# Performance work log

Measured on AMD Instinct MI355X. Metric: run time of the kernel, lower is better.

## Reference

```python
import jax, jax.numpy as jnp
import numpy as np

ALPHA = 1.0  # alpha hyperparameter; sigma=None and module in training mode with
# track_running_stats=True -> first-call behavior: sigma_square = alpha * mean(d2.detach())

def setup_inputs() -> dict:
    key = jax.random.key(0)
    X = jax.random.normal(key, (8192, 512), dtype=jnp.float32)
    return {"X": X}

def reference(X):
    # Pairwise squared L2 distances via ||xi||^2 + ||xj||^2 - 2 xi.xj (GEMM trick)
    sq = jnp.sum(X * X, axis=1)                      # [m]
    gram = X @ X.T                                   # [m, m]
    d2 = sq[:, None] + sq[None, :] - 2.0 * gram      # [m, m]
    d2 = jnp.maximum(d2, 0.0)                        # numerical safety
    sigma_square = ALPHA * jnp.mean(jax.lax.stop_gradient(d2))
    return jnp.exp(-d2 / (2.0 * sigma_square))
```

## Files before the change

kernel.cpp:

```cpp
#include <hip/hip_runtime.h>
#include <stdint.h>
#include <math.h>

#define MROWS 8192
#define KDIM  512

typedef __attribute__((ext_vector_type(8))) short short8;
typedef __attribute__((ext_vector_type(4))) float f32x4;

#if __has_builtin(__builtin_amdgcn_exp2f)
#define EXP2F(x) __builtin_amdgcn_exp2f(x)
#else
#define EXP2F(x) exp2f(x)
#endif

#define GL2LDS(gp, lp) __builtin_amdgcn_global_load_lds( \
    (__attribute__((address_space(1))) void*)(gp),       \
    (__attribute__((address_space(3))) void*)(lp), 16, 0, 0)

__device__ inline unsigned short f2bf_rne(float f) {
  unsigned u = __builtin_bit_cast(unsigned, f);
  unsigned r = 0x7FFFu + ((u >> 16) & 1u);
  return (unsigned short)((u + r) >> 16);
}

__device__ inline int swzP(int row, int g) {
  return (row * 4) ^ (g ^ (row & 3)) ^ (((row >> 2) & 1) << 2);
}

__global__ __launch_bounds__(512) void k_prep(
    const float* __restrict__ X, unsigned short* __restrict__ Xb,
    float* __restrict__ sq, float* __restrict__ svec_part,
    float* __restrict__ sumsq_part) {
  __shared__ float ssv[8][512];
  __shared__ float ssq[8];
  const int tid = threadIdx.x, lane = tid & 63, w = tid >> 6;
  const int b = blockIdx.x;

  float ca[8] = {0.f, 0.f, 0.f, 0.f, 0.f, 0.f, 0.f, 0.f};
  float lss = 0.f;

  for (int rr = 0; rr < 4; ++rr) {
    const int row = b * 32 + w * 4 + rr;
    const float4* xr = (const float4*)(X + (size_t)row * KDIM);
    float4 v0 = xr[lane];
    float4 v1 = xr[64 + lane];

    ushort4 p0, p1;
    p0.x = f2bf_rne(v0.x); p0.y = f2bf_rne(v0.y);
    p0.z = f2bf_rne(v0.z); p0.w = f2bf_rne(v0.w);
    p1.x = f2bf_rne(v1.x); p1.y = f2bf_rne(v1.y);
    p1.z = f2bf_rne(v1.z); p1.w = f2bf_rne(v1.w);
    *(ushort4*)(Xb + (size_t)row * KDIM + lane * 4)       = p0;
    *(ushort4*)(Xb + (size_t)row * KDIM + 256 + lane * 4) = p1;

    float s2 = v0.x*v0.x + v0.y*v0.y + v0.z*v0.z + v0.w*v0.w
             + v1.x*v1.x + v1.y*v1.y + v1.z*v1.z + v1.w*v1.w;
    float rs = s2;
#pragma unroll
    for (int off = 32; off; off >>= 1) rs += __shfl_xor(rs, off, 64);
    if (lane == 0) sq[row] = rs;
    lss += s2;

    ca[0] += v0.x; ca[1] += v0.y; ca[2] += v0.z; ca[3] += v0.w;
    ca[4] += v1.x; ca[5] += v1.y; ca[6] += v1.z; ca[7] += v1.w;
  }

#pragma unroll
  for (int i = 0; i < 4; ++i) {
    ssv[w][lane * 4 + i]       = ca[i];
    ssv[w][256 + lane * 4 + i] = ca[4 + i];
  }
  float wsum = lss;
#pragma unroll
  for (int off = 32; off; off >>= 1) wsum += __shfl_xor(wsum, off, 64);
  if (lane == 0) ssq[w] = wsum;
  __syncthreads();

  float s = 0.f;
#pragma unroll
  for (int ww = 0; ww < 8; ++ww) s += ssv[ww][tid];
  svec_part[(size_t)b * 512 + tid] = s;
  if (tid == 0)
    sumsq_part[b] = ssq[0] + ssq[1] + ssq[2] + ssq[3] +
                    ssq[4] + ssq[5] + ssq[6] + ssq[7];
}

__global__ __launch_bounds__(512) void k_sig_a(
    const float* __restrict__ svec_part, const float* __restrict__ sumsq_part,
    float* __restrict__ svec2, float* __restrict__ sumsq2) {
  const int tid = threadIdx.x, b = blockIdx.x;
  float s = 0.f;
#pragma unroll
  for (int k = 0; k < 4; ++k)
    s += svec_part[(size_t)(b * 4 + k) * 512 + tid];
  svec2[(size_t)b * 512 + tid] = s;
  if (tid == 0)
    sumsq2[b] = sumsq_part[b * 4] + sumsq_part[b * 4 + 1] +
                sumsq_part[b * 4 + 2] + sumsq_part[b * 4 + 3];
}

__global__ __launch_bounds__(256) void k_sigma(
    const float* __restrict__ svec2, const float* __restrict__ sumsq2,
    float* __restrict__ scale) {
  __shared__ float red[4];
  const int tid = threadIdx.x, lane = tid & 63, w = tid >> 6;
  float s1 = 0.f, s2 = 0.f;
#pragma unroll 4
  for (int b = 0; b < 64; ++b) {
    s1 += svec2[(size_t)b * 512 + tid];
    s2 += svec2[(size_t)b * 512 + 256 + tid];
  }
  float ss = s1 * s1 + s2 * s2;
#pragma unroll
  for (int off = 32; off; off >>= 1) ss += __shfl_xor(ss, off, 64);
  if (lane == 0) red[w] = ss;
  __syncthreads();
  if (tid == 0) {
    float sst = red[0] + red[1] + red[2] + red[3];
    float sumsq = 0.f;
#pragma unroll
    for (int b = 0; b < 64; ++b) sumsq += sumsq2[b];
    const float m = (float)MROWS;
    float meand2 = 2.f * sumsq / m - 2.f * sst / (m * m);
    float sigma2 = 1.0f * meand2;
    scale[0] = 1.4426950408889634f / (2.f * sigma2);
  }
}

__global__ __launch_bounds__(256, 3) void k_gemm(
    const unsigned short* __restrict__ Xb, const float* __restrict__ sq,
    const float* __restrict__ scale, float* __restrict__ out) {
  __shared__ __align__(16) char smem[49152];
  unsigned short* Asm = (unsigned short*)smem;
  unsigned short* Bsm = (unsigned short*)(smem + 24576);
  float* tr = (float*)smem;

  const int tid = threadIdx.x, lane = tid & 63, w = tid >> 6;
  const int wr = w >> 1, wc = w & 1;
  const int ln15 = lane & 15, g = lane >> 4;

  const int blk = blockIdx.x;
  const int r = (blk & 7) * 260 + (blk >> 3);
  int bi, bj;
  if (r < 1536) {
    const int sp = r >> 8;
    const int inner = r & 255;
    const int SI = (sp < 3) ? 0 : ((sp < 5) ? 1 : 2);
    const int SJ = (sp < 3) ? sp + 1 : ((sp < 5) ? sp - 1 : 3);
    bi = SI * 16 + (inner & 15);
    bj = SJ * 16 + (inner >> 4);
  } else {
    const int rd = r - 1536;
    const int sd = rd / 136;
    const int k = rd - sd * 136;
    int b = (int)((sqrtf(8.0f * (float)k + 1.0f) - 1.0f) * 0.5f);
    while ((b + 1) * (b + 2) / 2 <= k) ++b;
    while (b * (b + 1) / 2 > k) --b;
    const int a = k - b * (b + 1) / 2;
    bi = sd * 16 + a;
    bj = sd * 16 + b;
  }

  const unsigned short* XbA = Xb + (size_t)bi * 128 * KDIM;
  const unsigned short* XbB = Xb + (size_t)bj * 128 * KDIM;
  const unsigned short* sA[2];
  const unsigned short* sB[2];
  int dOf[2];
#pragma unroll
  for (int q = 0; q < 2; ++q) {
    const int P = (w << 7) + (q << 6) + lane;
    const int row = ((P >> 3) << 1) | (((P >> 2) ^ (P >> 4)) & 1);
    const int gg = (P & 3) ^ (row & 3);
    sA[q] = XbA + row * KDIM + gg * 8;
    sB[q] = XbB + row * KDIM + gg * 8;
    dOf[q] = (w << 10) + (q << 9);
  }

  int eaA[4], eaB[4];
#pragma unroll
  for (int m = 0; m < 4; ++m)
    eaA[m] = swzP(wr * 64 + m * 16 + ln15, g) * 8;
#pragma unroll
  for (int n = 0; n < 4; ++n)
    eaB[n] = swzP(wc * 64 + n * 16 + ln15, g) * 8;

  f32x4 acc[4][4] = {};
  short8 a[4], bfr[4];

#define STG_A(sb, kt)                                          \
  { GL2LDS(sA[0] + (kt) * 32, &Asm[(sb) * 4096 + dOf[0]]);     \
    GL2LDS(sA[1] + (kt) * 32, &Asm[(sb) * 4096 + dOf[1]]); }
#define STG_B(sb, kt)                                          \
  { GL2LDS(sB[0] + (kt) * 32, &Bsm[(sb) * 4096 + dOf[0]]);     \
    GL2LDS(sB[1] + (kt) * 32, &Bsm[(sb) * 4096 + dOf[1]]); }

  STG_A(0, 0); STG_B(0, 0);
  STG_A(1, 1); STG_B(1, 1);
  asm volatile("s_waitcnt vmcnt(4)" ::: "memory");
  __builtin_amdgcn_s_barrier();
  __builtin_amdgcn_sched_barrier(0);

#pragma unroll
  for (int i = 0; i < 16; ++i) {
    const int rb = i % 3;

#pragma unroll
    for (int m = 0; m < 4; ++m)
      a[m] = *(const short8*)&Asm[rb * 4096 + eaA[m]];
#pragma unroll
    for (int n = 0; n < 4; ++n)
      bfr[n] = *(const short8*)&Bsm[rb * 4096 + eaB[n]];

    if (i < 14) {
      const int sb = (i + 2) % 3;
      STG_A(sb, i + 2);
      STG_B(sb, i + 2);
    }

    asm volatile("s_waitcnt lgkmcnt(0)" ::: "memory");
    __builtin_amdgcn_sched_barrier(0);

    __builtin_amdgcn_s_setprio(1);
#pragma unroll
    for (int m = 0; m < 4; ++m)
#pragma unroll
      for (int n = 0; n < 4; ++n)
        acc[m][n] = __builtin_amdgcn_mfma_f32_16x16x32_bf16(
            a[m], bfr[n], acc[m][n], 0, 0, 0);
    __builtin_amdgcn_s_setprio(0);

    if (i < 14) {
      asm volatile("s_waitcnt vmcnt(4)" ::: "memory");
    } else if (i == 14) {
      asm volatile("s_waitcnt vmcnt(0)" ::: "memory");
    }
    __builtin_amdgcn_s_barrier();
    __builtin_amdgcn_sched_barrier(0);
  }

  asm volatile("s_waitcnt vmcnt(0) lgkmcnt(0)" ::: "memory");

  const float cs = scale[0];
  const int hi4 = g * 4;
  const int rbase = bi * 128 + wr * 64 + hi4;
  const int cbase = bj * 128 + wc * 64 + ln15;

  float scol[4];
#pragma unroll
  for (int n = 0; n < 4; ++n) scol[n] = sq[cbase + n * 16];

#pragma unroll
  for (int m = 0; m < 4; ++m) {
#pragma unroll
    for (int r2 = 0; r2 < 4; ++r2) {
      const float sr = sq[rbase + m * 16 + r2];
#pragma unroll
      for (int n = 0; n < 4; ++n) {
        float d2 = sr + scol[n] - 2.f * acc[m][n][r2];
        d2 = fmaxf(d2, 0.f);
        acc[m][n][r2] = EXP2F(-d2 * cs);
      }
    }
  }

#pragma unroll 1
  for (int c = 0; c < 2; ++c) {
    __syncthreads();
    if (wr == c) {
#pragma unroll
      for (int m = 0; m < 4; ++m)
#pragma unroll
        for (int n = 0; n < 4; ++n)
#pragma unroll
          for (int r2 = 0; r2 < 4; ++r2)
            tr[(m * 16 + hi4 + r2) * 132 + wc * 64 + n * 16 + ln15] =
                acc[m][n][r2];
    }
    __syncthreads();
#pragma unroll
    for (int rr = 0; rr < 8; ++rr) {
      const int row = w * 16 + rr * 2 + (lane >> 5);
      f32x4 v = *(const f32x4*)&tr[row * 132 + (lane & 31) * 4];
      __builtin_nontemporal_store(
          v, (f32x4*)&out[(size_t)(bi * 128 + c * 64 + row) * MROWS +
                          bj * 128 + (lane & 31) * 4]);
    }
  }

  if (bi != bj) {
#pragma unroll 1
    for (int cc = 0; cc < 2; ++cc) {
      __syncthreads();
      if (wc == cc) {
#pragma unroll
        for (int m = 0; m < 4; ++m) {
#pragma unroll
          for (int n = 0; n < 4; ++n) {
            const int c_loc = n * 16 + ln15;
            const int r_loc = wr * 64 + m * 16 + hi4;
            *(f32x4*)&tr[c_loc * 132 + r_loc] = acc[m][n];
          }
        }
      }
      __syncthreads();
#pragma unroll
      for (int rr = 0; rr < 8; ++rr) {
        const int row = w * 16 + rr * 2 + (lane >> 5);
        f32x4 v = *(const f32x4*)&tr[row * 132 + (lane & 31) * 4];
        __builtin_nontemporal_store(
            v, (f32x4*)&out[(size_t)(bj * 128 + cc * 64 + row) * MROWS +
                            bi * 128 + (lane & 31) * 4]);
      }
    }
  }
}

extern "C" void kernel_launch(void* const* d_in, const int* in_sizes, int n_in,
                              void* d_out, int out_size, void* d_ws,
                              size_t ws_size, hipStream_t stream) {
  (void)in_sizes; (void)n_in; (void)out_size; (void)ws_size;
  const float* X = (const float*)d_in[0];
  float* out = (float*)d_out;
  char* ws = (char*)d_ws;

  unsigned short* Xb  = (unsigned short*)ws;
  float* sq           = (float*)(ws + 8388608);
  float* svec_part    = (float*)(ws + 8421376);
  float* sumsq_part   = (float*)(ws + 8945664);
  float* svec2        = (float*)(ws + 8946688);
  float* sumsq2       = (float*)(ws + 9077760);
  float* scale        = (float*)(ws + 9078016);

  hipLaunchKernelGGL(k_prep, dim3(256), dim3(512), 0, stream,
                     X, Xb, sq, svec_part, sumsq_part);
  hipLaunchKernelGGL(k_sig_a, dim3(64), dim3(512), 0, stream,
                     svec_part, sumsq_part, svec2, sumsq2);
  hipLaunchKernelGGL(k_sigma, dim3(1), dim3(256), 0, stream,
                     svec2, sumsq2, scale);
  hipLaunchKernelGGL(k_gemm, dim3(2080), dim3(256), 0, stream,
                     Xb, sq, scale, out);
}
```

Before: 90.92 us.

## Shrink symmetric GEMM tiles to 64x64 with two-wave blocks

Changes the tiling from 128x128 tiles with four waves to 64x64 tiles with two waves per block. The tile schedule is rebuilt for 128 row blocks (8256 tiles) and the epilogue transposes through a smaller LDS buffer. The goal is more blocks, better load balance and higher occupancy from using less LDS per block. In exchange, operand reuse per byte loaded drops and twice as many tiles must fetch X.

After: 100.9 us. +11.0%, slower.

```diff
diff --git a/kernel.cpp b/kernel.cpp
--- a/kernel.cpp
+++ b/kernel.cpp
@@ -128,42 +128,43 @@
   }
 }
 
-__global__ __launch_bounds__(256, 3) void k_gemm(
+__global__ __launch_bounds__(128, 3) void k_gemm(
     const unsigned short* __restrict__ Xb, const float* __restrict__ sq,
     const float* __restrict__ scale, float* __restrict__ out) {
-  __shared__ __align__(16) char smem[49152];
+  __shared__ __align__(16) char smem[24576];
   unsigned short* Asm = (unsigned short*)smem;
-  unsigned short* Bsm = (unsigned short*)(smem + 24576);
+  unsigned short* Bsm = (unsigned short*)(smem + 12288);
   float* tr = (float*)smem;
 
   const int tid = threadIdx.x, lane = tid & 63, w = tid >> 6;
-  const int wr = w >> 1, wc = w & 1;
   const int ln15 = lane & 15, g = lane >> 4;
+  const int hi4 = g * 4;
 
   const int blk = blockIdx.x;
-  const int r = (blk & 7) * 260 + (blk >> 3);
+  const int r = (blk & 7) * 1032 + (blk >> 3);
   int bi, bj;
-  if (r < 1536) {
+  if (r < 7168) {
     const int sp = r >> 8;
     const int inner = r & 255;
-    const int SI = (sp < 3) ? 0 : ((sp < 5) ? 1 : 2);
-    const int SJ = (sp < 3) ? sp + 1 : ((sp < 5) ? sp - 1 : 3);
-    bi = SI * 16 + (inner & 15);
-    bj = SJ * 16 + (inner >> 4);
+    int si = 0, rem = sp;
+    while (rem >= 7 - si) { rem -= 7 - si; ++si; }
+    const int sj = si + 1 + rem;
+    bi = si * 16 + (inner & 15);
+    bj = sj * 16 + (inner >> 4);
   } else {
-    const int rd = r - 1536;
+    const int rd = r - 7168;
     const int sd = rd / 136;
     const int k = rd - sd * 136;
     int b = (int)((sqrtf(8.0f * (float)k + 1.0f) - 1.0f) * 0.5f);
     while ((b + 1) * (b + 2) / 2 <= k) ++b;
     while (b * (b + 1) / 2 > k) --b;
-    const int a = k - b * (b + 1) / 2;
-    bi = sd * 16 + a;
+    const int a2 = k - b * (b + 1) / 2;
+    bi = sd * 16 + a2;
     bj = sd * 16 + b;
   }
 
-  const unsigned short* XbA = Xb + (size_t)bi * 128 * KDIM;
-  const unsigned short* XbB = Xb + (size_t)bj * 128 * KDIM;
+  const unsigned short* XbA = Xb + (size_t)bi * 64 * KDIM;
+  const unsigned short* XbB = Xb + (size_t)bj * 64 * KDIM;
   const unsigned short* sA[2];
   const unsigned short* sB[2];
   int dOf[2];
@@ -177,23 +178,23 @@
     dOf[q] = (w << 10) + (q << 9);
   }
 
-  int eaA[4], eaB[4];
-#pragma unroll
-  for (int m = 0; m < 4; ++m)
-    eaA[m] = swzP(wr * 64 + m * 16 + ln15, g) * 8;
+  int eaA[2], eaB[4];
+#pragma unroll
+  for (int m = 0; m < 2; ++m)
+    eaA[m] = swzP(w * 32 + m * 16 + ln15, g) * 8;
 #pragma unroll
   for (int n = 0; n < 4; ++n)
-    eaB[n] = swzP(wc * 64 + n * 16 + ln15, g) * 8;
-
-  f32x4 acc[4][4] = {};
-  short8 a[4], bfr[4];
+    eaB[n] = swzP(n * 16 + ln15, g) * 8;
+
+  f32x4 acc[2][4] = {};
+  short8 a[2], bfr[4];
 
 #define STG_A(sb, kt)                                          \
-  { GL2LDS(sA[0] + (kt) * 32, &Asm[(sb) * 4096 + dOf[0]]);     \
-    GL2LDS(sA[1] + (kt) * 32, &Asm[(sb) * 4096 + dOf[1]]); }
+  { GL2LDS(sA[0] + (kt) * 32, &Asm[(sb) * 2048 + dOf[0]]);     \
+    GL2LDS(sA[1] + (kt) * 32, &Asm[(sb) * 2048 + dOf[1]]); }
 #define STG_B(sb, kt)                                          \
-  { GL2LDS(sB[0] + (kt) * 32, &Bsm[(sb) * 4096 + dOf[0]]);     \
-    GL2LDS(sB[1] + (kt) * 32, &Bsm[(sb) * 4096 + dOf[1]]); }
+  { GL2LDS(sB[0] + (kt) * 32, &Bsm[(sb) * 2048 + dOf[0]]);     \
+    GL2LDS(sB[1] + (kt) * 32, &Bsm[(sb) * 2048 + dOf[1]]); }
 
   STG_A(0, 0); STG_B(0, 0);
   STG_A(1, 1); STG_B(1, 1);
@@ -206,11 +207,11 @@
     const int rb = i % 3;
 
 #pragma unroll
-    for (int m = 0; m < 4; ++m)
-      a[m] = *(const short8*)&Asm[rb * 4096 + eaA[m]];
+    for (int m = 0; m < 2; ++m)
+      a[m] = *(const short8*)&Asm[rb * 2048 + eaA[m]];
 #pragma unroll
     for (int n = 0; n < 4; ++n)
-      bfr[n] = *(const short8*)&Bsm[rb * 4096 + eaB[n]];
+      bfr[n] = *(const short8*)&Bsm[rb * 2048 + eaB[n]];
 
     if (i < 14) {
       const int sb = (i + 2) % 3;
@@ -223,7 +224,7 @@
 
     __builtin_amdgcn_s_setprio(1);
 #pragma unroll
-    for (int m = 0; m < 4; ++m)
+    for (int m = 0; m < 2; ++m)
 #pragma unroll
       for (int n = 0; n < 4; ++n)
         acc[m][n] = __builtin_amdgcn_mfma_f32_16x16x32_bf16(
@@ -242,16 +243,15 @@
   asm volatile("s_waitcnt vmcnt(0) lgkmcnt(0)" ::: "memory");
 
   const float cs = scale[0];
-  const int hi4 = g * 4;
-  const int rbase = bi * 128 + wr * 64 + hi4;
-  const int cbase = bj * 128 + wc * 64 + ln15;
+  const int rbase = bi * 64 + w * 32 + hi4;
+  const int cbase = bj * 64 + ln15;
 
   float scol[4];
 #pragma unroll
   for (int n = 0; n < 4; ++n) scol[n] = sq[cbase + n * 16];
 
 #pragma unroll
-  for (int m = 0; m < 4; ++m) {
+  for (int m = 0; m < 2; ++m) {
 #pragma unroll
     for (int r2 = 0; r2 < 4; ++r2) {
       const float sr = sq[rbase + m * 16 + r2];
@@ -264,54 +264,41 @@
     }
   }
 
-#pragma unroll 1
-  for (int c = 0; c < 2; ++c) {
+  __syncthreads();
+#pragma unroll
+  for (int m = 0; m < 2; ++m)
+#pragma unroll
+    for (int n = 0; n < 4; ++n)
+#pragma unroll
+      for (int r2 = 0; r2 < 4; ++r2)
+        tr[(w * 32 + m * 16 + hi4 + r2) * 68 + n * 16 + ln15] =
+            acc[m][n][r2];
+  __syncthreads();
+#pragma unroll
+  for (int it = 0; it < 8; ++it) {
+    const int row = it * 8 + (tid >> 4);
+    f32x4 v = *(const f32x4*)&tr[row * 68 + (tid & 15) * 4];
+    __builtin_nontemporal_store(
+        v, (f32x4*)&out[(size_t)(bi * 64 + row) * MROWS +
+                        bj * 64 + (tid & 15) * 4]);
+  }
+
+  if (bi != bj) {
     __syncthreads();
-    if (wr == c) {
-#pragma unroll
-      for (int m = 0; m < 4; ++m)
-#pragma unroll
-        for (int n = 0; n < 4; ++n)
-#pragma unroll
-          for (int r2 = 0; r2 < 4; ++r2)
-            tr[(m * 16 + hi4 + r2) * 132 + wc * 64 + n * 16 + ln15] =
-                acc[m][n][r2];
-    }
+#pragma unroll
+    for (int m = 0; m < 2; ++m)
+#pragma unroll
+      for (int n = 0; n < 4; ++n)
+        *(f32x4*)&tr[(n * 16 + ln15) * 68 + w * 32 + m * 16 + hi4] =
+            acc[m][n];
     __syncthreads();
 #pragma unroll
-    for (int rr = 0; rr < 8; ++rr) {
-      const int row = w * 16 + rr * 2 + (lane >> 5);
-      f32x4 v = *(const f32x4*)&tr[row * 132 + (lane & 31) * 4];
+    for (int it = 0; it < 8; ++it) {
+      const int row = it * 8 + (tid >> 4);
+      f32x4 v = *(const f32x4*)&tr[row * 68 + (tid & 15) * 4];
       __builtin_nontemporal_store(
-          v, (f32x4*)&out[(size_t)(bi * 128 + c * 64 + row) * MROWS +
-                          bj * 128 + (lane & 31) * 4]);
-    }
-  }
-
-  if (bi != bj) {
-#pragma unroll 1
-    for (int cc = 0; cc < 2; ++cc) {
-      __syncthreads();
-      if (wc == cc) {
-#pragma unroll
-        for (int m = 0; m < 4; ++m) {
-#pragma unroll
-          for (int n = 0; n < 4; ++n) {
-            const int c_loc = n * 16 + ln15;
-            const int r_loc = wr * 64 + m * 16 + hi4;
-            *(f32x4*)&tr[c_loc * 132 + r_loc] = acc[m][n];
-          }
-        }
-      }
-      __syncthreads();
-#pragma unroll
-      for (int rr = 0; rr < 8; ++rr) {
-        const int row = w * 16 + rr * 2 + (lane >> 5);
-        f32x4 v = *(const f32x4*)&tr[row * 132 + (lane & 31) * 4];
-        __builtin_nontemporal_store(
-            v, (f32x4*)&out[(size_t)(bj * 128 + cc * 64 + row) * MROWS +
-                            bi * 128 + (lane & 31) * 4]);
-      }
+          v, (f32x4*)&out[(size_t)(bj * 64 + row) * MROWS +
+                          bi * 64 + (tid & 15) * 4]);
     }
   }
 }
@@ -338,6 +325,6 @@
                      svec_part, sumsq_part, svec2, sumsq2);
   hipLaunchKernelGGL(k_sigma, dim3(1), dim3(256), 0, stream,
                      svec2, sumsq2, scale);
-  hipLaunchKernelGGL(k_gemm, dim3(2080), dim3(256), 0, stream,
+  hipLaunchKernelGGL(k_gemm, dim3(8256), dim3(128), 0, stream,
                      Xb, sq, scale, out);
 }
```

## Make GEMM kernel persistent with a dedicated store wave for output writes

Applied to the files above, without the earlier changes.

Converts the GEMM-exp kernel into a persistent kernel of 512 blocks that loop over the 2080 triangular tiles. Each block gains a fifth wave that only copies the staged LDS tile out to global memory, while the four compute waves do the MFMA work. The LDS pipeline drops from triple to double buffering, and the transpose buffer gets its own separate region. The aim is to overlap the heavy output stores with the compute on the next tile, at the cost of more per-tile barriers, a larger LDS footprint and lower occupancy.

Measured after the change: 139.5 us. 53.4% more time.

```diff
diff --git a/kernel.cpp b/kernel.cpp
--- a/kernel.cpp
+++ b/kernel.cpp
@@ -17,6 +17,9 @@
 #define GL2LDS(gp, lp) __builtin_amdgcn_global_load_lds( \
     (__attribute__((address_space(1))) void*)(gp),       \
     (__attribute__((address_space(3))) void*)(lp), 16, 0, 0)
+
+#define BAR() do { __builtin_amdgcn_s_barrier(); \
+                   __builtin_amdgcn_sched_barrier(0); } while (0)
 
 __device__ inline unsigned short f2bf_rne(float f) {
   unsigned u = __builtin_bit_cast(unsigned, f);
@@ -128,65 +131,75 @@
   }
 }
 
-__global__ __launch_bounds__(256, 3) void k_gemm(
+__global__ __launch_bounds__(320) void k_gemm(
     const unsigned short* __restrict__ Xb, const float* __restrict__ sq,
     const float* __restrict__ scale, float* __restrict__ out) {
-  __shared__ __align__(16) char smem[49152];
+  __shared__ __align__(16) char smem[66560];
   unsigned short* Asm = (unsigned short*)smem;
-  unsigned short* Bsm = (unsigned short*)(smem + 24576);
-  float* tr = (float*)smem;
+  unsigned short* Bsm = (unsigned short*)(smem + 16384);
+  float* tr = (float*)(smem + 32768);
 
   const int tid = threadIdx.x, lane = tid & 63, w = tid >> 6;
-  const int wr = w >> 1, wc = w & 1;
+  const bool sw = (w == 4);
+  const int wr = (w >> 1) & 1, wc = w & 1;
   const int ln15 = lane & 15, g = lane >> 4;
+  const int hi4 = g * 4;
 
   const int blk = blockIdx.x;
-  const int r = (blk & 7) * 260 + (blk >> 3);
-  int bi, bj;
-  if (r < 1536) {
-    const int sp = r >> 8;
-    const int inner = r & 255;
-    const int SI = (sp < 3) ? 0 : ((sp < 5) ? 1 : 2);
-    const int SJ = (sp < 3) ? sp + 1 : ((sp < 5) ? sp - 1 : 3);
-    bi = SI * 16 + (inner & 15);
-    bj = SJ * 16 + (inner >> 4);
-  } else {
-    const int rd = r - 1536;
-    const int sd = rd / 136;
-    const int k = rd - sd * 136;
-    int b = (int)((sqrtf(8.0f * (float)k + 1.0f) - 1.0f) * 0.5f);
-    while ((b + 1) * (b + 2) / 2 <= k) ++b;
-    while (b * (b + 1) / 2 > k) --b;
-    const int a = k - b * (b + 1) / 2;
-    bi = sd * 16 + a;
-    bj = sd * 16 + b;
-  }
-
-  const unsigned short* XbA = Xb + (size_t)bi * 128 * KDIM;
-  const unsigned short* XbB = Xb + (size_t)bj * 128 * KDIM;
-  const unsigned short* sA[2];
-  const unsigned short* sB[2];
-  int dOf[2];
-#pragma unroll
-  for (int q = 0; q < 2; ++q) {
-    const int P = (w << 7) + (q << 6) + lane;
-    const int row = ((P >> 3) << 1) | (((P >> 2) ^ (P >> 4)) & 1);
-    const int gg = (P & 3) ^ (row & 3);
-    sA[q] = XbA + row * KDIM + gg * 8;
-    sB[q] = XbB + row * KDIM + gg * 8;
-    dOf[q] = (w << 10) + (q << 9);
-  }
-
-  int eaA[4], eaB[4];
-#pragma unroll
-  for (int m = 0; m < 4; ++m)
-    eaA[m] = swzP(wr * 64 + m * 16 + ln15, g) * 8;
-#pragma unroll
-  for (int n = 0; n < 4; ++n)
-    eaB[n] = swzP(wc * 64 + n * 16 + ln15, g) * 8;
-
-  f32x4 acc[4][4] = {};
-  short8 a[4], bfr[4];
+  const int perm = (blk & 7) * 64 + (blk >> 3);
+  const float cs = scale[0];
+
+#pragma unroll 1
+  for (int k = 0;; ++k) {
+    const int r = perm + k * 512;
+    if (r >= 2080) break;
+
+    int bi, bj;
+    if (r < 1536) {
+      const int sp = r >> 8;
+      const int inner = r & 255;
+      const int SI = (sp < 3) ? 0 : ((sp < 5) ? 1 : 2);
+      const int SJ = (sp < 3) ? sp + 1 : ((sp < 5) ? sp - 1 : 3);
+      bi = SI * 16 + (inner & 15);
+      bj = SJ * 16 + (inner >> 4);
+    } else {
+      const int rd = r - 1536;
+      const int sd = rd / 136;
+      const int kk = rd - sd * 136;
+      int b = (int)((sqrtf(8.0f * (float)kk + 1.0f) - 1.0f) * 0.5f);
+      while ((b + 1) * (b + 2) / 2 <= kk) ++b;
+      while (b * (b + 1) / 2 > kk) --b;
+      const int a2 = kk - b * (b + 1) / 2;
+      bi = sd * 16 + a2;
+      bj = sd * 16 + b;
+    }
+    const bool offdiag = (bi != bj);
+
+    const unsigned short* XbA = Xb + (size_t)bi * 128 * KDIM;
+    const unsigned short* XbB = Xb + (size_t)bj * 128 * KDIM;
+    const unsigned short* sA[2];
+    const unsigned short* sB[2];
+    int dOf[2];
+#pragma unroll
+    for (int q = 0; q < 2; ++q) {
+      const int P = ((w & 3) << 7) + (q << 6) + lane;
+      const int row = ((P >> 3) << 1) | (((P >> 2) ^ (P >> 4)) & 1);
+      const int gg = (P & 3) ^ (row & 3);
+      sA[q] = XbA + row * KDIM + gg * 8;
+      sB[q] = XbB + row * KDIM + gg * 8;
+      dOf[q] = ((w & 3) << 10) + (q << 9);
+    }
+
+    int eaA[4], eaB[4];
+#pragma unroll
+    for (int m = 0; m < 4; ++m)
+      eaA[m] = swzP(wr * 64 + m * 16 + ln15, g) * 8;
+#pragma unroll
+    for (int n = 0; n < 4; ++n)
+      eaB[n] = swzP(wc * 64 + n * 16 + ln15, g) * 8;
+
+    f32x4 acc[4][4] = {};
+    short8 a[4], bfr[4];
 
 #define STG_A(sb, kt)                                          \
   { GL2LDS(sA[0] + (kt) * 32, &Asm[(sb) * 4096 + dOf[0]]);     \
@@ -195,122 +208,120 @@
   { GL2LDS(sB[0] + (kt) * 32, &Bsm[(sb) * 4096 + dOf[0]]);     \
     GL2LDS(sB[1] + (kt) * 32, &Bsm[(sb) * 4096 + dOf[1]]); }
 
-  STG_A(0, 0); STG_B(0, 0);
-  STG_A(1, 1); STG_B(1, 1);
-  asm volatile("s_waitcnt vmcnt(4)" ::: "memory");
-  __builtin_amdgcn_s_barrier();
-  __builtin_amdgcn_sched_barrier(0);
-
-#pragma unroll
-  for (int i = 0; i < 16; ++i) {
-    const int rb = i % 3;
-
-#pragma unroll
-    for (int m = 0; m < 4; ++m)
-      a[m] = *(const short8*)&Asm[rb * 4096 + eaA[m]];
-#pragma unroll
-    for (int n = 0; n < 4; ++n)
-      bfr[n] = *(const short8*)&Bsm[rb * 4096 + eaB[n]];
-
-    if (i < 14) {
-      const int sb = (i + 2) % 3;
-      STG_A(sb, i + 2);
-      STG_B(sb, i + 2);
-    }
-
-    asm volatile("s_waitcnt lgkmcnt(0)" ::: "memory");
-    __builtin_amdgcn_sched_barrier(0);
-
-    __builtin_amdgcn_s_setprio(1);
-#pragma unroll
-    for (int m = 0; m < 4; ++m)
-#pragma unroll
-      for (int n = 0; n < 4; ++n)
-        acc[m][n] = __builtin_amdgcn_mfma_f32_16x16x32_bf16(
-            a[m], bfr[n], acc[m][n], 0, 0, 0);
-    __builtin_amdgcn_s_setprio(0);
-
-    if (i < 14) {
-      asm volatile("s_waitcnt vmcnt(4)" ::: "memory");
-    } else if (i == 14) {
+    if (!sw) {
+      STG_A(0, 0); STG_B(0, 0);
       asm volatile("s_waitcnt vmcnt(0)" ::: "memory");
     }
-    __builtin_amdgcn_s_barrier();
-    __builtin_amdgcn_sched_barrier(0);
-  }
-
-  asm volatile("s_waitcnt vmcnt(0) lgkmcnt(0)" ::: "memory");
-
-  const float cs = scale[0];
-  const int hi4 = g * 4;
-  const int rbase = bi * 128 + wr * 64 + hi4;
-  const int cbase = bj * 128 + wc * 64 + ln15;
-
-  float scol[4];
-#pragma unroll
-  for (int n = 0; n < 4; ++n) scol[n] = sq[cbase + n * 16];
-
-#pragma unroll
-  for (int m = 0; m < 4; ++m) {
-#pragma unroll
-    for (int r2 = 0; r2 < 4; ++r2) {
-      const float sr = sq[rbase + m * 16 + r2];
-#pragma unroll
-      for (int n = 0; n < 4; ++n) {
-        float d2 = sr + scol[n] - 2.f * acc[m][n][r2];
-        d2 = fmaxf(d2, 0.f);
-        acc[m][n][r2] = EXP2F(-d2 * cs);
-      }
-    }
-  }
+    BAR();
+
+#pragma unroll
+    for (int i = 0; i < 16; ++i) {
+      const int rb = i & 1;
+      if (!sw) {
+        if (i < 15) { STG_A(rb ^ 1, i + 1); STG_B(rb ^ 1, i + 1); }
+#pragma unroll
+        for (int m = 0; m < 4; ++m)
+          a[m] = *(const short8*)&Asm[rb * 4096 + eaA[m]];
+#pragma unroll
+        for (int n = 0; n < 4; ++n)
+          bfr[n] = *(const short8*)&Bsm[rb * 4096 + eaB[n]];
+        asm volatile("s_waitcnt lgkmcnt(0)" ::: "memory");
+        __builtin_amdgcn_sched_barrier(0);
+        __builtin_amdgcn_s_setprio(1);
+#pragma unroll
+        for (int m = 0; m < 4; ++m)
+#pragma unroll
+          for (int n = 0; n < 4; ++n)
+            acc[m][n] = __builtin_amdgcn_mfma_f32_16x16x32_bf16(
+                a[m], bfr[n], acc[m][n], 0, 0, 0);
+        __builtin_amdgcn_s_setprio(0);
+        asm volatile("s_waitcnt vmcnt(0)" ::: "memory");
+      }
+      BAR();
+    }
+
+    if (!sw) {
+      const int rbase = bi * 128 + wr * 64 + hi4;
+      const int cbase = bj * 128 + wc * 64 + ln15;
+      float scol[4];
+#pragma unroll
+      for (int n = 0; n < 4; ++n) scol[n] = sq[cbase + n * 16];
+#pragma unroll
+      for (int m = 0; m < 4; ++m) {
+#pragma unroll
+        for (int r2 = 0; r2 < 4; ++r2) {
+          const float sr = sq[rbase + m * 16 + r2];
+#pragma unroll
+          for (int n = 0; n < 4; ++n) {
+            float d2 = sr + scol[n] - 2.f * acc[m][n][r2];
+            d2 = fmaxf(d2, 0.f);
+            acc[m][n][r2] = EXP2F(-d2 * cs);
+          }
+        }
+      }
+    }
 
 #pragma unroll 1
-  for (int c = 0; c < 2; ++c) {
-    __syncthreads();
-    if (wr == c) {
-#pragma unroll
-      for (int m = 0; m < 4; ++m)
-#pragma unroll
-        for (int n = 0; n < 4; ++n)
-#pragma unroll
-          for (int r2 = 0; r2 < 4; ++r2)
-            tr[(m * 16 + hi4 + r2) * 132 + wc * 64 + n * 16 + ln15] =
-                acc[m][n][r2];
-    }
-    __syncthreads();
-#pragma unroll
-    for (int rr = 0; rr < 8; ++rr) {
-      const int row = w * 16 + rr * 2 + (lane >> 5);
-      f32x4 v = *(const f32x4*)&tr[row * 132 + (lane & 31) * 4];
-      __builtin_nontemporal_store(
-          v, (f32x4*)&out[(size_t)(bi * 128 + c * 64 + row) * MROWS +
-                          bj * 128 + (lane & 31) * 4]);
-    }
-  }
-
-  if (bi != bj) {
+    for (int c = 0; c < 2; ++c) {
+      if (!sw) {
+        if (wr == c) {
+#pragma unroll
+          for (int m = 0; m < 4; ++m)
+#pragma unroll
+            for (int n = 0; n < 4; ++n)
+#pragma unroll
+              for (int r2 = 0; r2 < 4; ++r2)
+                tr[(m * 16 + hi4 + r2) * 132 + wc * 64 + n * 16 + ln15] =
+                    acc[m][n][r2];
+        }
+        asm volatile("s_waitcnt lgkmcnt(0)" ::: "memory");
+      }
+      BAR();
+      if (sw) {
+        const size_t orow0 = (size_t)(bi * 128 + c * 64);
+        const size_t ocol0 = (size_t)(bj * 128);
+#pragma unroll
+        for (int k2 = 0; k2 < 32; ++k2) {
+          const int row = k2 * 2 + (lane >> 5);
+          f32x4 v = *(const f32x4*)&tr[row * 132 + (lane & 31) * 4];
+          __builtin_nontemporal_store(
+              v, (f32x4*)&out[(orow0 + row) * MROWS + ocol0 +
+                              (lane & 31) * 4]);
+        }
+        asm volatile("s_waitcnt lgkmcnt(0)" ::: "memory");
+      }
+      BAR();
+    }
+
+    if (offdiag) {
 #pragma unroll 1
-    for (int cc = 0; cc < 2; ++cc) {
-      __syncthreads();
-      if (wc == cc) {
-#pragma unroll
-        for (int m = 0; m < 4; ++m) {
-#pragma unroll
-          for (int n = 0; n < 4; ++n) {
-            const int c_loc = n * 16 + ln15;
-            const int r_loc = wr * 64 + m * 16 + hi4;
-            *(f32x4*)&tr[c_loc * 132 + r_loc] = acc[m][n];
+      for (int cc = 0; cc < 2; ++cc) {
+        if (!sw) {
+          if (wc == cc) {
+#pragma unroll
+            for (int m = 0; m < 4; ++m)
+#pragma unroll
+              for (int n = 0; n < 4; ++n)
+                *(f32x4*)&tr[(n * 16 + ln15) * 132 + wr * 64 + m * 16 + hi4] =
+                    acc[m][n];
           }
-        }
-      }
-      __syncthreads();
-#pragma unroll
-      for (int rr = 0; rr < 8; ++rr) {
-        const int row = w * 16 + rr * 2 + (lane >> 5);
-        f32x4 v = *(const f32x4*)&tr[row * 132 + (lane & 31) * 4];
-        __builtin_nontemporal_store(
-            v, (f32x4*)&out[(size_t)(bj * 128 + cc * 64 + row) * MROWS +
-                            bi * 128 + (lane & 31) * 4]);
+          asm volatile("s_waitcnt lgkmcnt(0)" ::: "memory");
+        }
+        BAR();
+        if (sw) {
+          const size_t orow0 = (size_t)(bj * 128 + cc * 64);
+          const size_t ocol0 = (size_t)(bi * 128);
+#pragma unroll
+          for (int k2 = 0; k2 < 32; ++k2) {
+            const int row = k2 * 2 + (lane >> 5);
+            f32x4 v = *(const f32x4*)&tr[row * 132 + (lane & 31) * 4];
+            __builtin_nontemporal_store(
+                v, (f32x4*)&out[(orow0 + row) * MROWS + ocol0 +
+                                (lane & 31) * 4]);
+          }
+          asm volatile("s_waitcnt lgkmcnt(0)" ::: "memory");
+        }
+        BAR();
       }
     }
   }
@@ -338,6 +349,6 @@
                      svec_part, sumsq_part, svec2, sumsq2);
   hipLaunchKernelGGL(k_sigma, dim3(1), dim3(256), 0, stream,
                      svec2, sumsq2, scale);
-  hipLaunchKernelGGL(k_gemm, dim3(2080), dim3(256), 0, stream,
+  hipLaunchKernelGGL(k_gemm, dim3(512), dim3(320), 0, stream,
                      Xb, sq, scale, out);
 }
```

## Load GEMM fragments directly from global memory into registers, bypassing LDS

Applied to the files above, without the earlier changes.

Replaces the triple-buffered global_load_lds staging with swizzled LDS reads by direct per-lane global loads of bf16 fragments into registers, double-buffered across K steps. This removes LDS traffic, barriers and waitcnt synchronisation from the main loop and shrinks shared memory to just the epilogue transpose buffer. In exchange each wave reloads its own operand rows from global/L2 with no sharing across waves, the 16-byte loads are strided by row, and register pressure rises from holding two fragment sets.

Measured after the change: 181.3 us. 99.5% more time.

```diff
diff --git a/kernel.cpp b/kernel.cpp
--- a/kernel.cpp
+++ b/kernel.cpp
@@ -14,18 +14,10 @@
 #define EXP2F(x) exp2f(x)
 #endif
 
-#define GL2LDS(gp, lp) __builtin_amdgcn_global_load_lds( \
-    (__attribute__((address_space(1))) void*)(gp),       \
-    (__attribute__((address_space(3))) void*)(lp), 16, 0, 0)
-
 __device__ inline unsigned short f2bf_rne(float f) {
   unsigned u = __builtin_bit_cast(unsigned, f);
   unsigned r = 0x7FFFu + ((u >> 16) & 1u);
   return (unsigned short)((u + r) >> 16);
-}
-
-__device__ inline int swzP(int row, int g) {
-  return (row * 4) ^ (g ^ (row & 3)) ^ (((row >> 2) & 1) << 2);
 }
 
 __global__ __launch_bounds__(512) void k_prep(
@@ -131,14 +123,12 @@
 __global__ __launch_bounds__(256, 3) void k_gemm(
     const unsigned short* __restrict__ Xb, const float* __restrict__ sq,
     const float* __restrict__ scale, float* __restrict__ out) {
-  __shared__ __align__(16) char smem[49152];
-  unsigned short* Asm = (unsigned short*)smem;
-  unsigned short* Bsm = (unsigned short*)(smem + 24576);
-  float* tr = (float*)smem;
+  __shared__ __align__(16) float tr[64 * 132];
 
   const int tid = threadIdx.x, lane = tid & 63, w = tid >> 6;
   const int wr = w >> 1, wc = w & 1;
   const int ln15 = lane & 15, g = lane >> 4;
+  const int hi4 = g * 4;
 
   const int blk = blockIdx.x;
   const int r = (blk & 7) * 260 + (blk >> 3);
@@ -157,92 +147,49 @@
     int b = (int)((sqrtf(8.0f * (float)k + 1.0f) - 1.0f) * 0.5f);
     while ((b + 1) * (b + 2) / 2 <= k) ++b;
     while (b * (b + 1) / 2 > k) --b;
-    const int a = k - b * (b + 1) / 2;
-    bi = sd * 16 + a;
+    const int a2 = k - b * (b + 1) / 2;
+    bi = sd * 16 + a2;
     bj = sd * 16 + b;
   }
 
-  const unsigned short* XbA = Xb + (size_t)bi * 128 * KDIM;
-  const unsigned short* XbB = Xb + (size_t)bj * 128 * KDIM;
-  const unsigned short* sA[2];
-  const unsigned short* sB[2];
-  int dOf[2];
-#pragma unroll
-  for (int q = 0; q < 2; ++q) {
-    const int P = (w << 7) + (q << 6) + lane;
-    const int row = ((P >> 3) << 1) | (((P >> 2) ^ (P >> 4)) & 1);
-    const int gg = (P & 3) ^ (row & 3);
-    sA[q] = XbA + row * KDIM + gg * 8;
-    sB[q] = XbB + row * KDIM + gg * 8;
-    dOf[q] = (w << 10) + (q << 9);
-  }
-
-  int eaA[4], eaB[4];
+  const unsigned short* ap[4];
+  const unsigned short* bp[4];
 #pragma unroll
   for (int m = 0; m < 4; ++m)
-    eaA[m] = swzP(wr * 64 + m * 16 + ln15, g) * 8;
+    ap[m] = Xb + (size_t)(bi * 128 + wr * 64 + m * 16 + ln15) * KDIM + g * 8;
 #pragma unroll
   for (int n = 0; n < 4; ++n)
-    eaB[n] = swzP(wc * 64 + n * 16 + ln15, g) * 8;
+    bp[n] = Xb + (size_t)(bj * 128 + wc * 64 + n * 16 + ln15) * KDIM + g * 8;
 
   f32x4 acc[4][4] = {};
-  short8 a[4], bfr[4];
-
-#define STG_A(sb, kt)                                          \
-  { GL2LDS(sA[0] + (kt) * 32, &Asm[(sb) * 4096 + dOf[0]]);     \
-    GL2LDS(sA[1] + (kt) * 32, &Asm[(sb) * 4096 + dOf[1]]); }
-#define STG_B(sb, kt)                                          \
-  { GL2LDS(sB[0] + (kt) * 32, &Bsm[(sb) * 4096 + dOf[0]]);     \
-    GL2LDS(sB[1] + (kt) * 32, &Bsm[(sb) * 4096 + dOf[1]]); }
-
-  STG_A(0, 0); STG_B(0, 0);
-  STG_A(1, 1); STG_B(1, 1);
-  asm volatile("s_waitcnt vmcnt(4)" ::: "memory");
-  __builtin_amdgcn_s_barrier();
-  __builtin_amdgcn_sched_barrier(0);
-
-#pragma unroll
-  for (int i = 0; i < 16; ++i) {
-    const int rb = i % 3;
-
-#pragma unroll
-    for (int m = 0; m < 4; ++m)
-      a[m] = *(const short8*)&Asm[rb * 4096 + eaA[m]];
-#pragma unroll
-    for (int n = 0; n < 4; ++n)
-      bfr[n] = *(const short8*)&Bsm[rb * 4096 + eaB[n]];
-
-    if (i < 14) {
-      const int sb = (i + 2) % 3;
-      STG_A(sb, i + 2);
-      STG_B(sb, i + 2);
-    }
-
-    asm volatile("s_waitcnt lgkmcnt(0)" ::: "memory");
-    __builtin_amdgcn_sched_barrier(0);
-
-    __builtin_amdgcn_s_setprio(1);
-#pragma unroll
-    for (int m = 0; m < 4; ++m)
-#pragma unroll
-      for (int n = 0; n < 4; ++n)
-        acc[m][n] = __builtin_amdgcn_mfma_f32_16x16x32_bf16(
-            a[m], bfr[n], acc[m][n], 0, 0, 0);
-    __builtin_amdgcn_s_setprio(0);
-
-    if (i < 14) {
-      asm volatile("s_waitcnt vmcnt(4)" ::: "memory");
-    } else if (i == 14) {
-      asm volatile("s_waitcnt vmcnt(0)" ::: "memory");
-    }
-    __builtin_amdgcn_s_barrier();
-    __builtin_amdgcn_sched_barrier(0);
-  }
-
-  asm volatile("s_waitcnt vmcnt(0) lgkmcnt(0)" ::: "memory");
+  short8 a0[4], b0[4], a1[4], b1[4];
+
+#define LOADF(AR, BR, i)                                        \
+  { _Pragma("unroll")                                           \
+    for (int m = 0; m < 4; ++m)                                 \
+      AR[m] = *(const short8*)(ap[m] + (i) * 32);               \
+    _Pragma("unroll")                                           \
+    for (int n = 0; n < 4; ++n)                                 \
+      BR[n] = *(const short8*)(bp[n] + (i) * 32); }
+
+#define MFMAS(AR, BR)                                           \
+  { _Pragma("unroll")                                           \
+    for (int m = 0; m < 4; ++m)                                 \
+      _Pragma("unroll")                                         \
+      for (int n = 0; n < 4; ++n)                               \
+        acc[m][n] = __builtin_amdgcn_mfma_f32_16x16x32_bf16(    \
+            AR[m], BR[n], acc[m][n], 0, 0, 0); }
+
+  LOADF(a0, b0, 0);
+#pragma unroll
+  for (int i = 0; i < 16; i += 2) {
+    if (i + 1 < 16) LOADF(a1, b1, i + 1);
+    MFMAS(a0, b0);
+    if (i + 2 < 16) LOADF(a0, b0, i + 2);
+    MFMAS(a1, b1);
+  }
 
   const float cs = scale[0];
-  const int hi4 = g * 4;
   const int rbase = bi * 128 + wr * 64 + hi4;
   const int cbase = bj * 128 + wc * 64 + ln15;
 
```
